# Kernel optimization log

Hardware: AMD Instinct MI355X
Metric: run time of the kernel (lower is better)

## Reference

```python
import jax, jax.numpy as jnp
import numpy as np

N_NODES = 100000   # n_nodes
N_EDGES = 1600000  # n_nodes * avg_degree(16)
D_IN = 128
D_OUT = 128


def setup_inputs() -> dict:
    key = jax.random.key(0)
    k1, k2, k3, k4, k5 = jax.random.split(key, 5)
    h = jax.random.normal(k1, (N_NODES, D_IN), dtype=jnp.float32)
    edge_src = jax.random.randint(k2, (N_EDGES,), 0, N_NODES, dtype=jnp.int32)
    edge_dst = jax.random.randint(k3, (N_EDGES,), 0, N_NODES, dtype=jnp.int32)
    # Linear params, init per reset_parameters: U(-stdv, stdv), stdv = 1/sqrt(in_feats)
    stdv = 1.0 / np.sqrt(D_IN)
    W = jax.random.uniform(k4, (D_OUT, D_IN), dtype=jnp.float32, minval=-stdv, maxval=stdv)
    b = jax.random.uniform(k5, (D_OUT,), dtype=jnp.float32, minval=-stdv, maxval=stdv)
    return {"h": h, "edge_src": edge_src, "edge_dst": edge_dst, "W": W, "b": b}


def reference(h, edge_src, edge_dst, W, b):
    # update_all(copy_src('h'), sum) == neighbor-sum aggregation (SpMM with 0/1 adjacency)
    ah = jax.ops.segment_sum(h[edge_src], edge_dst, num_segments=N_NODES)  # [N, D_IN]
    # dense linear + activation fused on the aggregated features
    return jax.nn.relu(ah @ W.T + b)  # [N, D_OUT]
```

## Files before the change

### kernel.cpp

```cpp
#include <hip/hip_runtime.h>

#define D 128
#define BKT_SHIFT 9
#define BKT_SIZE 512
#define P1_EPB 4096
#define SW_LDU 68

typedef __attribute__((ext_vector_type(8))) short bf16x8;
typedef __attribute__((ext_vector_type(4))) float f32x4;

__device__ inline unsigned int pack2bf(float a, float b) {
    unsigned int ua = __float_as_uint(a);
    unsigned int ub = __float_as_uint(b);
    ua = (ua + 0x7fffu + ((ua >> 16) & 1u)) >> 16;
    ub = (ub + 0x7fffu + ((ub >> 16) & 1u)) >> 16;
    return ua | (ub << 16);
}
__device__ inline unsigned short pack1bf(float a) {
    unsigned int ua = __float_as_uint(a);
    return (unsigned short)((ua + 0x7fffu + ((ua >> 16) & 1u)) >> 16);
}


__global__ __launch_bounds__(256) void p1_partition_kernel(
    const int* __restrict__ esrc, const int* __restrict__ edst,
    int* __restrict__ bucketCur, unsigned int* __restrict__ pairs,
    int n_edges, int cap)
{
    __shared__ int hist[256];
    __shared__ int lbase[256];
    __shared__ int gbase[256];
    __shared__ int cur[256];
    __shared__ unsigned int buf[P1_EPB];
    __shared__ unsigned char bkt8[P1_EPB];
    const int tid = threadIdx.x;
    const int base = blockIdx.x * P1_EPB;
    hist[tid] = 0;
    __syncthreads();
    unsigned int pk[16]; int bk[16];
    #pragma unroll
    for (int k = 0; k < 16; k++) {
        int e = base + k * 256 + tid;
        if (e < n_edges) {
            int sv = esrc[e], dv = edst[e];
            bk[k] = dv >> BKT_SHIFT;
            pk[k] = ((unsigned)sv << BKT_SHIFT) | (unsigned)(dv & (BKT_SIZE - 1));
            atomicAdd(&hist[bk[k]], 1);
        } else bk[k] = -1;
    }
    __syncthreads();
    const int v = hist[tid];
    if (v > 0) {
        int res = atomicAdd(&bucketCur[tid], v);
        if (res > cap) res = cap;
        gbase[tid] = tid * cap + res;
    }
    lbase[tid] = v;
    __syncthreads();
    #pragma unroll
    for (int off = 1; off < 256; off <<= 1) {
        int x = (tid >= off) ? lbase[tid - off] : 0;
        __syncthreads();
        lbase[tid] += x;
        __syncthreads();
    }
    const int excl = lbase[tid] - v;
    __syncthreads();
    lbase[tid] = excl;
    cur[tid] = excl;
    __syncthreads();
    #pragma unroll
    for (int k = 0; k < 16; k++) {
        if (bk[k] >= 0) {
            int loc = atomicAdd(&cur[bk[k]], 1);
            buf[loc] = pk[k];
            bkt8[loc] = (unsigned char)bk[k];
        }
    }
    __syncthreads();
    const int total = min(P1_EPB, n_edges - base);
    for (int i = tid; i < total; i += 256) {
        int b = bkt8[i];
        pairs[(size_t)gbase[b] + (i - lbase[b])] = buf[i];
    }
}

__global__ __launch_bounds__(256) void p2_sort_gemm_kernel(
    const unsigned int* __restrict__ pairs, const int* __restrict__ bucketCur,
    int* __restrict__ sorted_src, int* __restrict__ gstart, int* __restrict__ gend,
    const float* __restrict__ h, const float* __restrict__ W,
    unsigned short* __restrict__ z,
    int n_nodes, int nbk, int cap)
{
    __shared__ union SU {
        struct { int hist[BKT_SIZE]; int cur[BKT_SIZE]; int sb[256]; } s;
        unsigned int sW[128 * SW_LDU];
    } u;
    const int tid = threadIdx.x;

    if ((int)blockIdx.x < nbk) {
        const int bkt = blockIdx.x;
        const int nbase = bkt << BKT_SHIFT;
        const int pstart = bkt * cap;
        int cnt = bucketCur[bkt];
        if (cnt > cap) cnt = cap;
        const int pend = pstart + cnt;
        u.s.hist[tid] = 0; u.s.hist[tid + 256] = 0;
        __syncthreads();
        {
            int j = pstart + tid;
            for (; j + 768 < pend; j += 1024) {
                unsigned int q0 = pairs[j];
                unsigned int q1 = pairs[j + 256];
                unsigned int q2 = pairs[j + 512];
                unsigned int q3 = pairs[j + 768];
                atomicAdd(&u.s.hist[q0 & (BKT_SIZE - 1)], 1);
                atomicAdd(&u.s.hist[q1 & (BKT_SIZE - 1)], 1);
                atomicAdd(&u.s.hist[q2 & (BKT_SIZE - 1)], 1);
                atomicAdd(&u.s.hist[q3 & (BKT_SIZE - 1)], 1);
            }
            for (; j < pend; j += 256)
                atomicAdd(&u.s.hist[pairs[j] & (BKT_SIZE - 1)], 1);
        }
        __syncthreads();
        int a  = u.s.hist[2 * tid];
        int b2 = u.s.hist[2 * tid + 1];
        int psum = a + b2;
        u.s.sb[tid] = psum;
        __syncthreads();
        #pragma unroll
        for (int off = 1; off < 256; off <<= 1) {
            int x = (tid >= off) ? u.s.sb[tid - off] : 0;
            __syncthreads();
            u.s.sb[tid] += x;
            __syncthreads();
        }
        int pexcl = u.s.sb[tid] - psum;
        u.s.cur[2 * tid] = pexcl;
        u.s.cur[2 * tid + 1] = pexcl + a;
        __syncthreads();
        for (int i = tid; i < BKT_SIZE; i += 256) {
            int nd = nbase + i;
            if (nd < n_nodes) {
                int st = pstart + u.s.cur[i];
                gstart[nd] = st;
                gend[nd] = st + u.s.hist[i];
            }
        }
        __syncthreads();
        {
            int j = pstart + tid;
            for (; j + 768 < pend; j += 1024) {
                unsigned int q0 = pairs[j];
                unsigned int q1 = pairs[j + 256];
                unsigned int q2 = pairs[j + 512];
                unsigned int q3 = pairs[j + 768];
                int p0 = pstart + atomicAdd(&u.s.cur[q0 & (BKT_SIZE - 1)], 1);
                int p1 = pstart + atomicAdd(&u.s.cur[q1 & (BKT_SIZE - 1)], 1);
                int p2 = pstart + atomicAdd(&u.s.cur[q2 & (BKT_SIZE - 1)], 1);
                int p3 = pstart + atomicAdd(&u.s.cur[q3 & (BKT_SIZE - 1)], 1);
                sorted_src[p0] = (int)(q0 >> BKT_SHIFT);
                sorted_src[p1] = (int)(q1 >> BKT_SHIFT);
                sorted_src[p2] = (int)(q2 >> BKT_SHIFT);
                sorted_src[p3] = (int)(q3 >> BKT_SHIFT);
            }
            for (; j < pend; j += 256) {
                unsigned int p = pairs[j];
                int local = p & (BKT_SIZE - 1);
                int pos = pstart + atomicAdd(&u.s.cur[local], 1);
                sorted_src[pos] = (int)(p >> BKT_SHIFT);
            }
        }
    } else {
        const int gbid = blockIdx.x - nbk;
        for (int i = tid; i < 4096; i += 256) {
            float4 w = ((const float4*)W)[i];
            int row = i >> 5, c4 = i & 31;
            unsigned int* dst = &u.sW[row * SW_LDU + c4 * 2];
            dst[0] = pack2bf(w.x, w.y);
            dst[1] = pack2bf(w.z, w.w);
        }
        __syncthreads();

        const int wave = tid >> 6;
        const int lane = tid & 63;
        const int m = lane & 15;
        const int q = lane >> 4;
        const int r0 = gbid * 64 + wave * 16;
        const int arow = r0 + m;
        const bool rvalid = arow < n_nodes;

        bf16x8 afrag[4];
        #pragma unroll
        for (int ks = 0; ks < 4; ks++) {
            float4 x = make_float4(0.f, 0.f, 0.f, 0.f), y = x;
            if (rvalid) {
                const float4* p = (const float4*)(h + (size_t)arow * D + ks * 32 + q * 8);
                x = p[0]; y = p[1];
            }
            union { unsigned int uu[4]; bf16x8 v; } cvt;
            cvt.uu[0] = pack2bf(x.x, x.y);
            cvt.uu[1] = pack2bf(x.z, x.w);
            cvt.uu[2] = pack2bf(y.x, y.y);
            cvt.uu[3] = pack2bf(y.z, y.w);
            afrag[ks] = cvt.v;
        }

        f32x4 acc[8];
        #pragma unroll
        for (int ct = 0; ct < 8; ct++) acc[ct] = (f32x4){0.f, 0.f, 0.f, 0.f};

        #pragma unroll
        for (int ct = 0; ct < 8; ct++) {
            #pragma unroll
            for (int ks = 0; ks < 4; ks++) {
                const unsigned int* p = &u.sW[(ct * 16 + m) * SW_LDU + ks * 16 + q * 4];
                union { uint4 uu; bf16x8 v; } bu;
                bu.uu = *(const uint4*)p;
                acc[ct] = __builtin_amdgcn_mfma_f32_16x16x32_bf16(afrag[ks], bu.v, acc[ct], 0, 0, 0);
            }
        }

        __syncthreads();
        unsigned short* lds_us = (unsigned short*)u.sW;
        #pragma unroll
        for (int ct = 0; ct < 8; ct++) {
            #pragma unroll
            for (int i = 0; i < 4; i++) {
                lds_us[(wave * 16 + q * 4 + i) * 130 + ct * 16 + m] = pack1bf(acc[ct][i]);
            }
        }
        __syncthreads();
        const unsigned int* lds32 = (const unsigned int*)u.sW;
        const int r0blk = gbid * 64;
        #pragma unroll
        for (int pass = 0; pass < 4; pass++) {
            int idx = pass * 256 + tid;
            int row = idx >> 4;
            int c16 = idx & 15;
            int r = r0blk + row;
            if (r < n_nodes) {
                int bo = row * 65 + c16 * 4;
                uint4 val;
                val.x = lds32[bo]; val.y = lds32[bo + 1];
                val.z = lds32[bo + 2]; val.w = lds32[bo + 3];
                ((uint4*)z)[(size_t)r * 16 + c16] = val;
            }
        }
    }
}

__global__ __launch_bounds__(256) void gather_row_kernel(
    const unsigned short* __restrict__ z, const int* __restrict__ gstart,
    const int* __restrict__ gend, const int* __restrict__ sorted_src,
    const float* __restrict__ b, float* __restrict__ out, int n_nodes)
{
    const int tid = threadIdx.x;
    const int node = blockIdx.x * 16 + (tid >> 4);
    const int lane = tid & 15;
    if (node >= n_nodes) return;
    int e = gstart[node];
    const int end = gend[node];
    const uint4* __restrict__ z4 = (const uint4*)z;
    float acc[8];
    #pragma unroll
    for (int i = 0; i < 8; i++) acc[i] = 0.f;
#define ADDV(v) do { \
    acc[0] += __uint_as_float((v).x << 16); acc[1] += __uint_as_float((v).x & 0xffff0000u); \
    acc[2] += __uint_as_float((v).y << 16); acc[3] += __uint_as_float((v).y & 0xffff0000u); \
    acc[4] += __uint_as_float((v).z << 16); acc[5] += __uint_as_float((v).z & 0xffff0000u); \
    acc[6] += __uint_as_float((v).w << 16); acc[7] += __uint_as_float((v).w & 0xffff0000u); } while (0)
    for (; e + 4 <= end; e += 4) {
        int s0 = sorted_src[e + 0];
        int s1 = sorted_src[e + 1];
        int s2 = sorted_src[e + 2];
        int s3 = sorted_src[e + 3];
        uint4 v0 = z4[(size_t)s0 * 16 + lane];
        uint4 v1 = z4[(size_t)s1 * 16 + lane];
        uint4 v2 = z4[(size_t)s2 * 16 + lane];
        uint4 v3 = z4[(size_t)s3 * 16 + lane];
        ADDV(v0); ADDV(v1); ADDV(v2); ADDV(v3);
    }
    for (; e < end; e++) {
        uint4 v = z4[(size_t)sorted_src[e] * 16 + lane];
        ADDV(v);
    }
#undef ADDV
    float4 b0 = ((const float4*)b)[lane * 2];
    float4 b1 = ((const float4*)b)[lane * 2 + 1];
    float4* o = (float4*)(out + (size_t)node * D + lane * 8);
    o[0] = make_float4(fmaxf(acc[0] + b0.x, 0.f), fmaxf(acc[1] + b0.y, 0.f),
                       fmaxf(acc[2] + b0.z, 0.f), fmaxf(acc[3] + b0.w, 0.f));
    o[1] = make_float4(fmaxf(acc[4] + b1.x, 0.f), fmaxf(acc[5] + b1.y, 0.f),
                       fmaxf(acc[6] + b1.z, 0.f), fmaxf(acc[7] + b1.w, 0.f));
}


__global__ __launch_bounds__(256) void scatter_kernel(
    const float* __restrict__ h, const int* __restrict__ esrc,
    const int* __restrict__ edst, float* __restrict__ out, int n_edges)
{
    int gid = blockIdx.x * 256 + threadIdx.x;
    int e = gid >> 5;
    int l = gid & 31;
    if (e >= n_edges) return;
    int s = esrc[e];
    int d = edst[e];
    float4 v = ((const float4*)(h + (size_t)s * D))[l];
    float* o = out + (size_t)d * D + (size_t)l * 4;
    atomicAdd(o + 0, v.x);
    atomicAdd(o + 1, v.y);
    atomicAdd(o + 2, v.z);
    atomicAdd(o + 3, v.w);
}

__global__ __launch_bounds__(256) void mfma_gemm_relu_kernel(
    float* __restrict__ io, const float* __restrict__ W,
    const float* __restrict__ b, int n_nodes)
{
    __shared__ unsigned int sW[128 * SW_LDU];
    const int tid = threadIdx.x;
    for (int i = tid; i < 4096; i += 256) {
        float4 w = ((const float4*)W)[i];
        int row = i >> 5, c4 = i & 31;
        unsigned int* dst = &sW[row * SW_LDU + c4 * 2];
        dst[0] = pack2bf(w.x, w.y);
        dst[1] = pack2bf(w.z, w.w);
    }
    __syncthreads();
    const int wave = tid >> 6;
    const int lane = tid & 63;
    const int m = lane & 15;
    const int q = lane >> 4;
    const int r0 = blockIdx.x * 64 + wave * 16;
    const int arow = r0 + m;
    const bool rvalid = arow < n_nodes;
    bf16x8 afrag[4];
    #pragma unroll
    for (int ks = 0; ks < 4; ks++) {
        float4 x = make_float4(0.f, 0.f, 0.f, 0.f), y = x;
        if (rvalid) {
            const float4* p = (const float4*)(io + (size_t)arow * D + ks * 32 + q * 8);
            x = p[0]; y = p[1];
        }
        union { unsigned int u[4]; bf16x8 v; } cvt;
        cvt.u[0] = pack2bf(x.x, x.y);
        cvt.u[1] = pack2bf(x.z, x.w);
        cvt.u[2] = pack2bf(y.x, y.y);
        cvt.u[3] = pack2bf(y.z, y.w);
        afrag[ks] = cvt.v;
    }
    f32x4 acc[8];
    #pragma unroll
    for (int ct = 0; ct < 8; ct++) acc[ct] = (f32x4){0.f, 0.f, 0.f, 0.f};
    #pragma unroll
    for (int ct = 0; ct < 8; ct++) {
        #pragma unroll
        for (int ks = 0; ks < 4; ks++) {
            const unsigned int* p = &sW[(ct * 16 + m) * SW_LDU + ks * 16 + q * 4];
            union { uint4 u; bf16x8 v; } bu;
            bu.u = *(const uint4*)p;
            acc[ct] = __builtin_amdgcn_mfma_f32_16x16x32_bf16(afrag[ks], bu.v, acc[ct], 0, 0, 0);
        }
    }
    #pragma unroll
    for (int ct = 0; ct < 8; ct++) {
        int col = ct * 16 + m;
        float bias = b[col];
        #pragma unroll
        for (int i = 0; i < 4; i++) {
            int r = r0 + q * 4 + i;
            if (r < n_nodes) {
                float v = acc[ct][i] + bias;
                io[(size_t)r * D + col] = v > 0.f ? v : 0.f;
            }
        }
    }
}

extern "C" void kernel_launch(void* const* d_in, const int* in_sizes, int n_in,
                              void* d_out, int out_size, void* d_ws, size_t ws_size,
                              hipStream_t stream) {
    const float* h    = (const float*)d_in[0];
    const int*   esrc = (const int*)d_in[1];
    const int*   edst = (const int*)d_in[2];
    const float* W    = (const float*)d_in[3];
    const float* b    = (const float*)d_in[4];
    float* out = (float*)d_out;
    const int n_nodes = in_sizes[0] / D;
    const int n_edges = in_sizes[1];
    const int NBK = (n_nodes + BKT_SIZE - 1) / BKT_SIZE;

    const int avg = (n_edges + NBK - 1) / NBK;
    const int CAP = (2 * avg + 2047) & ~2047;
    const size_t win = (size_t)NBK * CAP;

    size_t fixed = ((size_t)2 * n_nodes + NBK + 2 * win) * 4;
    size_t z_off = (fixed + 15) & ~(size_t)15;
    size_t need = z_off + (size_t)n_nodes * D * 2;

    if (ws_size >= need && NBK <= 256 && n_nodes <= (1 << 22)) {
        int* gstart     = (int*)d_ws;
        int* gend       = gstart + n_nodes;
        int* bucketCur  = gend + n_nodes;
        int* sorted_src = bucketCur + NBK;
        unsigned int* pairs = (unsigned int*)(sorted_src + win);
        unsigned short* z   = (unsigned short*)((char*)d_ws + z_off);

        hipMemsetAsync(bucketCur, 0, (size_t)NBK * sizeof(int), stream);
        p1_partition_kernel<<<(n_edges + P1_EPB - 1) / P1_EPB, 256, 0, stream>>>(
            esrc, edst, bucketCur, pairs, n_edges, CAP);
        const int gemmBlocks = (n_nodes + 63) / 64;
        p2_sort_gemm_kernel<<<NBK + gemmBlocks, 256, 0, stream>>>(
            pairs, bucketCur, sorted_src, gstart, gend, h, W, z,
            n_nodes, NBK, CAP);
        gather_row_kernel<<<(n_nodes + 15) / 16, 256, 0, stream>>>(
            z, gstart, gend, sorted_src, b, out, n_nodes);
        return;
    }

    hipMemsetAsync(out, 0, (size_t)n_nodes * D * sizeof(float), stream);
    long long total = (long long)n_edges * 32;
    scatter_kernel<<<(int)((total + 255) / 256), 256, 0, stream>>>(h, esrc, edst, out, n_edges);
    mfma_gemm_relu_kernel<<<(n_nodes + 63) / 64, 256, 0, stream>>>(out, W, b, n_nodes);
}
```

Before: 223.3 us.

## Fuse partition, sort/GEMM and gather into one cooperative persistent kernel

Replaces the memset plus three separate kernel launches with a single cooperative persistent kernel that uses grid-wide syncs between the partition, bucket-sort/GEMM and gather phases, with atomic work counters for dynamic scheduling. The aim is to remove launch gaps and tail effects between the stages. In exchange, the grid is limited to resident blocks, the shared-memory union may lower occupancy, and grid.sync adds its own barrier cost. A fallback to the old multi-kernel path remains if cooperative launch is unavailable.

After: 495.5 us. +121.8%, slower.

```diff
diff --git a/kernel.cpp b/kernel.cpp
--- a/kernel.cpp
+++ b/kernel.cpp
@@ -1,4 +1,7 @@
 #include <hip/hip_runtime.h>
+#include <hip/hip_cooperative_groups.h>
+
+namespace cg = cooperative_groups;
 
 #define D 128
 #define BKT_SHIFT 9
@@ -19,6 +22,298 @@
 __device__ inline unsigned short pack1bf(float a) {
     unsigned int ua = __float_as_uint(a);
     return (unsigned short)((ua + 0x7fffu + ((ua >> 16) & 1u)) >> 16);
+}
+
+
+union MegaLDS {
+    struct { int hist[256]; int lbase[256]; int gbase[256]; int cur[256];
+             unsigned int buf[P1_EPB]; unsigned char bkt8[P1_EPB]; } p1;
+    struct { int hist[BKT_SIZE]; int cur[BKT_SIZE]; int sb[256]; } s;
+    unsigned int sW[128 * SW_LDU];
+};
+
+__global__ void mega_kernel(
+    const int* __restrict__ esrc, const int* __restrict__ edst,
+    const float* __restrict__ h, const float* __restrict__ W,
+    const float* __restrict__ b, float* __restrict__ out,
+    int* __restrict__ bucketCur, int* __restrict__ gstart,
+    int* __restrict__ gend, int* __restrict__ sorted_src,
+    unsigned int* __restrict__ pairs, unsigned short* __restrict__ z,
+    int* __restrict__ counters,
+    int n_nodes, int n_edges, int nbk, int cap, int nchunks,
+    int gemmBlocks, int nGather)
+{
+    cg::grid_group grid = cg::this_grid();
+    __shared__ MegaLDS u;
+    __shared__ int s_item;
+    const int tid = threadIdx.x;
+
+    if (blockIdx.x == 0) {
+        if (tid < nbk) bucketCur[tid] = 0;
+        if (tid < 16) counters[tid] = 0;
+    }
+    grid.sync();
+
+    for (int c = blockIdx.x; c < nchunks; c += gridDim.x) {
+        const int base = c * P1_EPB;
+        u.p1.hist[tid] = 0;
+        __syncthreads();
+        unsigned int pk[16]; int bk[16];
+        #pragma unroll
+        for (int k = 0; k < 16; k++) {
+            int e = base + k * 256 + tid;
+            if (e < n_edges) {
+                int sv = esrc[e], dv = edst[e];
+                bk[k] = dv >> BKT_SHIFT;
+                pk[k] = ((unsigned)sv << BKT_SHIFT) | (unsigned)(dv & (BKT_SIZE - 1));
+                atomicAdd(&u.p1.hist[bk[k]], 1);
+            } else bk[k] = -1;
+        }
+        __syncthreads();
+        const int v = u.p1.hist[tid];
+        if (v > 0) {
+            int res = atomicAdd(&bucketCur[tid], v);
+            if (res > cap) res = cap;
+            u.p1.gbase[tid] = tid * cap + res;
+        }
+        u.p1.lbase[tid] = v;
+        __syncthreads();
+        #pragma unroll
+        for (int off = 1; off < 256; off <<= 1) {
+            int x = (tid >= off) ? u.p1.lbase[tid - off] : 0;
+            __syncthreads();
+            u.p1.lbase[tid] += x;
+            __syncthreads();
+        }
+        const int excl = u.p1.lbase[tid] - v;
+        __syncthreads();
+        u.p1.lbase[tid] = excl;
+        u.p1.cur[tid] = excl;
+        __syncthreads();
+        #pragma unroll
+        for (int k = 0; k < 16; k++) {
+            if (bk[k] >= 0) {
+                int loc = atomicAdd(&u.p1.cur[bk[k]], 1);
+                u.p1.buf[loc] = pk[k];
+                u.p1.bkt8[loc] = (unsigned char)bk[k];
+            }
+        }
+        __syncthreads();
+        const int total = min(P1_EPB, n_edges - base);
+        for (int i = tid; i < total; i += 256) {
+            int bb = u.p1.bkt8[i];
+            pairs[(size_t)u.p1.gbase[bb] + (i - u.p1.lbase[bb])] = u.p1.buf[i];
+        }
+        __syncthreads();
+    }
+    grid.sync();
+
+    const int nItems2 = nbk + gemmBlocks;
+    while (true) {
+        __syncthreads();
+        if (tid == 0) s_item = atomicAdd(&counters[0], 1);
+        __syncthreads();
+        const int it = s_item;
+        if (it >= nItems2) break;
+
+        if (it < nbk) {
+            const int bkt = it;
+            const int nbase = bkt << BKT_SHIFT;
+            const int pstart = bkt * cap;
+            int cnt = bucketCur[bkt];
+            if (cnt > cap) cnt = cap;
+            const int pend = pstart + cnt;
+            u.s.hist[tid] = 0; u.s.hist[tid + 256] = 0;
+            __syncthreads();
+            {
+                int j = pstart + tid;
+                for (; j + 768 < pend; j += 1024) {
+                    unsigned int q0 = pairs[j];
+                    unsigned int q1 = pairs[j + 256];
+                    unsigned int q2 = pairs[j + 512];
+                    unsigned int q3 = pairs[j + 768];
+                    atomicAdd(&u.s.hist[q0 & (BKT_SIZE - 1)], 1);
+                    atomicAdd(&u.s.hist[q1 & (BKT_SIZE - 1)], 1);
+                    atomicAdd(&u.s.hist[q2 & (BKT_SIZE - 1)], 1);
+                    atomicAdd(&u.s.hist[q3 & (BKT_SIZE - 1)], 1);
+                }
+                for (; j < pend; j += 256)
+                    atomicAdd(&u.s.hist[pairs[j] & (BKT_SIZE - 1)], 1);
+            }
+            __syncthreads();
+            int a  = u.s.hist[2 * tid];
+            int b2 = u.s.hist[2 * tid + 1];
+            int psum = a + b2;
+            u.s.sb[tid] = psum;
+            __syncthreads();
+            #pragma unroll
+            for (int off = 1; off < 256; off <<= 1) {
+                int x = (tid >= off) ? u.s.sb[tid - off] : 0;
+                __syncthreads();
+                u.s.sb[tid] += x;
+                __syncthreads();
+            }
+            int pexcl = u.s.sb[tid] - psum;
+            u.s.cur[2 * tid] = pexcl;
+            u.s.cur[2 * tid + 1] = pexcl + a;
+            __syncthreads();
+            for (int i = tid; i < BKT_SIZE; i += 256) {
+                int nd = nbase + i;
+                if (nd < n_nodes) {
+                    int st = pstart + u.s.cur[i];
+                    gstart[nd] = st;
+                    gend[nd] = st + u.s.hist[i];
+                }
+            }
+            __syncthreads();
+            {
+                int j = pstart + tid;
+                for (; j + 768 < pend; j += 1024) {
+                    unsigned int q0 = pairs[j];
+                    unsigned int q1 = pairs[j + 256];
+                    unsigned int q2 = pairs[j + 512];
+                    unsigned int q3 = pairs[j + 768];
+                    int p0 = pstart + atomicAdd(&u.s.cur[q0 & (BKT_SIZE - 1)], 1);
+                    int p1 = pstart + atomicAdd(&u.s.cur[q1 & (BKT_SIZE - 1)], 1);
+                    int p2 = pstart + atomicAdd(&u.s.cur[q2 & (BKT_SIZE - 1)], 1);
+                    int p3 = pstart + atomicAdd(&u.s.cur[q3 & (BKT_SIZE - 1)], 1);
+                    sorted_src[p0] = (int)(q0 >> BKT_SHIFT);
+                    sorted_src[p1] = (int)(q1 >> BKT_SHIFT);
+                    sorted_src[p2] = (int)(q2 >> BKT_SHIFT);
+                    sorted_src[p3] = (int)(q3 >> BKT_SHIFT);
+                }
+                for (; j < pend; j += 256) {
+                    unsigned int p = pairs[j];
+                    int local = p & (BKT_SIZE - 1);
+                    int pos = pstart + atomicAdd(&u.s.cur[local], 1);
+                    sorted_src[pos] = (int)(p >> BKT_SHIFT);
+                }
+            }
+        } else {
+            const int gbid = it - nbk;
+            for (int i = tid; i < 4096; i += 256) {
+                float4 w = ((const float4*)W)[i];
+                int row = i >> 5, c4 = i & 31;
+                unsigned int* dst = &u.sW[row * SW_LDU + c4 * 2];
+                dst[0] = pack2bf(w.x, w.y);
+                dst[1] = pack2bf(w.z, w.w);
+            }
+            __syncthreads();
+
+            const int wave = tid >> 6;
+            const int lane = tid & 63;
+            const int m = lane & 15;
+            const int q = lane >> 4;
+            const int r0 = gbid * 64 + wave * 16;
+            const int arow = r0 + m;
+            const bool rvalid = arow < n_nodes;
+
+            bf16x8 afrag[4];
+            #pragma unroll
+            for (int ks = 0; ks < 4; ks++) {
+                float4 x = make_float4(0.f, 0.f, 0.f, 0.f), y = x;
+                if (rvalid) {
+                    const float4* p = (const float4*)(h + (size_t)arow * D + ks * 32 + q * 8);
+                    x = p[0]; y = p[1];
+                }
+                union { unsigned int uu[4]; bf16x8 v; } cvt;
+                cvt.uu[0] = pack2bf(x.x, x.y);
+                cvt.uu[1] = pack2bf(x.z, x.w);
+                cvt.uu[2] = pack2bf(y.x, y.y);
+                cvt.uu[3] = pack2bf(y.z, y.w);
+                afrag[ks] = cvt.v;
+            }
+
+            f32x4 acc[8];
+            #pragma unroll
+            for (int ct = 0; ct < 8; ct++) acc[ct] = (f32x4){0.f, 0.f, 0.f, 0.f};
+
+            #pragma unroll
+            for (int ct = 0; ct < 8; ct++) {
+                #pragma unroll
+                for (int ks = 0; ks < 4; ks++) {
+                    const unsigned int* p = &u.sW[(ct * 16 + m) * SW_LDU + ks * 16 + q * 4];
+                    union { uint4 uu; bf16x8 v; } bu;
+                    bu.uu = *(const uint4*)p;
+                    acc[ct] = __builtin_amdgcn_mfma_f32_16x16x32_bf16(afrag[ks], bu.v, acc[ct], 0, 0, 0);
+                }
+            }
+
+            __syncthreads();
+            unsigned short* lds_us = (unsigned short*)u.sW;
+            #pragma unroll
+            for (int ct = 0; ct < 8; ct++) {
+                #pragma unroll
+                for (int i = 0; i < 4; i++) {
+                    lds_us[(wave * 16 + q * 4 + i) * 130 + ct * 16 + m] = pack1bf(acc[ct][i]);
+                }
+            }
+            __syncthreads();
+            const unsigned int* lds32 = (const unsigned int*)u.sW;
+            const int r0blk = gbid * 64;
+            #pragma unroll
+            for (int pass = 0; pass < 4; pass++) {
+                int idx = pass * 256 + tid;
+                int row = idx >> 4;
+                int c16 = idx & 15;
+                int r = r0blk + row;
+                if (r < n_nodes) {
+                    int bo = row * 65 + c16 * 4;
+                    uint4 val;
+                    val.x = lds32[bo]; val.y = lds32[bo + 1];
+                    val.z = lds32[bo + 2]; val.w = lds32[bo + 3];
+                    ((uint4*)z)[(size_t)r * 16 + c16] = val;
+                }
+            }
+        }
+    }
+    grid.sync();
+
+    const uint4* __restrict__ z4 = (const uint4*)z;
+    while (true) {
+        __syncthreads();
+        if (tid == 0) s_item = atomicAdd(&counters[8], 1);
+        __syncthreads();
+        const int it = s_item;
+        if (it >= nGather) break;
+        const int node = it * 16 + (tid >> 4);
+        const int lane = tid & 15;
+        if (node < n_nodes) {
+            int e = gstart[node];
+            const int end = gend[node];
+            float acc[8];
+            #pragma unroll
+            for (int i = 0; i < 8; i++) acc[i] = 0.f;
+#define ADDV(v) do { \
+    acc[0] += __uint_as_float((v).x << 16); acc[1] += __uint_as_float((v).x & 0xffff0000u); \
+    acc[2] += __uint_as_float((v).y << 16); acc[3] += __uint_as_float((v).y & 0xffff0000u); \
+    acc[4] += __uint_as_float((v).z << 16); acc[5] += __uint_as_float((v).z & 0xffff0000u); \
+    acc[6] += __uint_as_float((v).w << 16); acc[7] += __uint_as_float((v).w & 0xffff0000u); } while (0)
+            for (; e + 4 <= end; e += 4) {
+                int s0 = sorted_src[e + 0];
+                int s1 = sorted_src[e + 1];
+                int s2 = sorted_src[e + 2];
+                int s3 = sorted_src[e + 3];
+                uint4 v0 = z4[(size_t)s0 * 16 + lane];
+                uint4 v1 = z4[(size_t)s1 * 16 + lane];
+                uint4 v2 = z4[(size_t)s2 * 16 + lane];
+                uint4 v3 = z4[(size_t)s3 * 16 + lane];
+                ADDV(v0); ADDV(v1); ADDV(v2); ADDV(v3);
+            }
+            for (; e < end; e++) {
+                uint4 v = z4[(size_t)sorted_src[e] * 16 + lane];
+                ADDV(v);
+            }
+#undef ADDV
+            float4 b0 = ((const float4*)b)[lane * 2];
+            float4 b1 = ((const float4*)b)[lane * 2 + 1];
+            float4* o = (float4*)(out + (size_t)node * D + lane * 8);
+            o[0] = make_float4(fmaxf(acc[0] + b0.x, 0.f), fmaxf(acc[1] + b0.y, 0.f),
+                               fmaxf(acc[2] + b0.z, 0.f), fmaxf(acc[3] + b0.w, 0.f));
+            o[1] = make_float4(fmaxf(acc[4] + b1.x, 0.f), fmaxf(acc[5] + b1.y, 0.f),
+                               fmaxf(acc[6] + b1.z, 0.f), fmaxf(acc[7] + b1.w, 0.f));
+        }
+    }
 }
 
 
@@ -390,12 +685,13 @@
     const int n_nodes = in_sizes[0] / D;
     const int n_edges = in_sizes[1];
     const int NBK = (n_nodes + BKT_SIZE - 1) / BKT_SIZE;
+    const int nchunks = (n_edges + P1_EPB - 1) / P1_EPB;
 
     const int avg = (n_edges + NBK - 1) / NBK;
     const int CAP = (2 * avg + 2047) & ~2047;
     const size_t win = (size_t)NBK * CAP;
 
-    size_t fixed = ((size_t)2 * n_nodes + NBK + 2 * win) * 4;
+    size_t fixed = ((size_t)2 * n_nodes + NBK + 16 + 2 * win) * 4;
     size_t z_off = (fixed + 15) & ~(size_t)15;
     size_t need = z_off + (size_t)n_nodes * D * 2;
 
@@ -403,18 +699,57 @@
         int* gstart     = (int*)d_ws;
         int* gend       = gstart + n_nodes;
         int* bucketCur  = gend + n_nodes;
-        int* sorted_src = bucketCur + NBK;
+        int* counters   = bucketCur + NBK;
+        int* sorted_src = counters + 16;
         unsigned int* pairs = (unsigned int*)(sorted_src + win);
         unsigned short* z   = (unsigned short*)((char*)d_ws + z_off);
 
+        const int gemmBlocks = (n_nodes + 63) / 64;
+        const int nGather = (n_nodes + 15) / 16;
+
+        static int s_coop_grid = -2;
+        if (s_coop_grid == -2) {
+            int nb = 0;
+            hipError_t err = hipOccupancyMaxActiveBlocksPerMultiprocessor(
+                &nb, (const void*)mega_kernel, 256, 0);
+            if (err != hipSuccess || nb < 1) {
+                s_coop_grid = -1;
+            } else {
+                hipDeviceProp_t prop{};
+                int dev = 0;
+                if (hipGetDevice(&dev) == hipSuccess &&
+                    hipGetDeviceProperties(&prop, dev) == hipSuccess &&
+                    prop.multiProcessorCount > 0 &&
+                    prop.cooperativeLaunch)
+                    s_coop_grid = nb * prop.multiProcessorCount;
+                else
+                    s_coop_grid = -1;
+            }
+        }
+
+        if (s_coop_grid >= 64) {
+            int grid = s_coop_grid > 4096 ? 4096 : s_coop_grid;
+            int ne = n_edges, nn = n_nodes, nb = NBK, cp = CAP, nc = nchunks;
+            int gb = gemmBlocks, ng = nGather;
+            void* args[] = {
+                (void*)&esrc, (void*)&edst, (void*)&h, (void*)&W, (void*)&b,
+                (void*)&out, (void*)&bucketCur, (void*)&gstart, (void*)&gend,
+                (void*)&sorted_src, (void*)&pairs, (void*)&z, (void*)&counters,
+                (void*)&nn, (void*)&ne, (void*)&nb, (void*)&cp, (void*)&nc,
+                (void*)&gb, (void*)&ng };
+            if (hipLaunchCooperativeKernel((void*)mega_kernel, dim3(grid),
+                                           dim3(256), args, 0, stream) == hipSuccess)
+                return;
+            s_coop_grid = -1;
+        }
+
         hipMemsetAsync(bucketCur, 0, (size_t)NBK * sizeof(int), stream);
-        p1_partition_kernel<<<(n_edges + P1_EPB - 1) / P1_EPB, 256, 0, stream>>>(
+        p1_partition_kernel<<<nchunks, 256, 0, stream>>>(
             esrc, edst, bucketCur, pairs, n_edges, CAP);
-        const int gemmBlocks = (n_nodes + 63) / 64;
         p2_sort_gemm_kernel<<<NBK + gemmBlocks, 256, 0, stream>>>(
             pairs, bucketCur, sorted_src, gstart, gend, h, W, z,
             n_nodes, NBK, CAP);
-        gather_row_kernel<<<(n_nodes + 15) / 16, 256, 0, stream>>>(
+        gather_row_kernel<<<nGather, 256, 0, stream>>>(
             z, gstart, gend, sorted_src, b, out, n_nodes);
         return;
     }
```

## Co-schedule GEMM with edge partition instead of bucket sort kernel

Applied to the files above, without the earlier changes.

Moves the dense h·W GEMM blocks from the bucket-sort kernel into the edge-partition kernel, and makes the per-bucket counting sort a separate kernel. Stage 2 had only ~196 sort blocks, so the GEMM work now overlaps with the ~391 partition chunks while the sort kernel runs alone. The shared-memory union now covers the partition buffers and the W tile, which may change occupancy. Partition blocks (4096 edges each) and GEMM blocks now compete for compute units in the same launch.

New measurement: 222.7 us. Within noise of the previous version (-0.3%).

```diff
diff --git a/kernel.cpp b/kernel.cpp
--- a/kernel.cpp
+++ b/kernel.cpp
@@ -22,157 +22,72 @@
 }
 
 
-__global__ __launch_bounds__(256) void p1_partition_kernel(
+__global__ __launch_bounds__(256) void p1_gemm_kernel(
     const int* __restrict__ esrc, const int* __restrict__ edst,
     int* __restrict__ bucketCur, unsigned int* __restrict__ pairs,
-    int n_edges, int cap)
-{
-    __shared__ int hist[256];
-    __shared__ int lbase[256];
-    __shared__ int gbase[256];
-    __shared__ int cur[256];
-    __shared__ unsigned int buf[P1_EPB];
-    __shared__ unsigned char bkt8[P1_EPB];
-    const int tid = threadIdx.x;
-    const int base = blockIdx.x * P1_EPB;
-    hist[tid] = 0;
-    __syncthreads();
-    unsigned int pk[16]; int bk[16];
-    #pragma unroll
-    for (int k = 0; k < 16; k++) {
-        int e = base + k * 256 + tid;
-        if (e < n_edges) {
-            int sv = esrc[e], dv = edst[e];
-            bk[k] = dv >> BKT_SHIFT;
-            pk[k] = ((unsigned)sv << BKT_SHIFT) | (unsigned)(dv & (BKT_SIZE - 1));
-            atomicAdd(&hist[bk[k]], 1);
-        } else bk[k] = -1;
-    }
-    __syncthreads();
-    const int v = hist[tid];
-    if (v > 0) {
-        int res = atomicAdd(&bucketCur[tid], v);
-        if (res > cap) res = cap;
-        gbase[tid] = tid * cap + res;
-    }
-    lbase[tid] = v;
-    __syncthreads();
-    #pragma unroll
-    for (int off = 1; off < 256; off <<= 1) {
-        int x = (tid >= off) ? lbase[tid - off] : 0;
-        __syncthreads();
-        lbase[tid] += x;
-        __syncthreads();
-    }
-    const int excl = lbase[tid] - v;
-    __syncthreads();
-    lbase[tid] = excl;
-    cur[tid] = excl;
-    __syncthreads();
-    #pragma unroll
-    for (int k = 0; k < 16; k++) {
-        if (bk[k] >= 0) {
-            int loc = atomicAdd(&cur[bk[k]], 1);
-            buf[loc] = pk[k];
-            bkt8[loc] = (unsigned char)bk[k];
-        }
-    }
-    __syncthreads();
-    const int total = min(P1_EPB, n_edges - base);
-    for (int i = tid; i < total; i += 256) {
-        int b = bkt8[i];
-        pairs[(size_t)gbase[b] + (i - lbase[b])] = buf[i];
-    }
-}
-
-__global__ __launch_bounds__(256) void p2_sort_gemm_kernel(
-    const unsigned int* __restrict__ pairs, const int* __restrict__ bucketCur,
-    int* __restrict__ sorted_src, int* __restrict__ gstart, int* __restrict__ gend,
     const float* __restrict__ h, const float* __restrict__ W,
     unsigned short* __restrict__ z,
-    int n_nodes, int nbk, int cap)
+    int n_edges, int n_nodes, int nchunks, int cap)
 {
-    __shared__ union SU {
-        struct { int hist[BKT_SIZE]; int cur[BKT_SIZE]; int sb[256]; } s;
+    __shared__ union U {
+        struct { int hist[256]; int lbase[256]; int gbase[256]; int cur[256];
+                 unsigned int buf[P1_EPB]; unsigned char bkt8[P1_EPB]; } p1;
         unsigned int sW[128 * SW_LDU];
     } u;
     const int tid = threadIdx.x;
 
-    if ((int)blockIdx.x < nbk) {
-        const int bkt = blockIdx.x;
-        const int nbase = bkt << BKT_SHIFT;
-        const int pstart = bkt * cap;
-        int cnt = bucketCur[bkt];
-        if (cnt > cap) cnt = cap;
-        const int pend = pstart + cnt;
-        u.s.hist[tid] = 0; u.s.hist[tid + 256] = 0;
-        __syncthreads();
-        {
-            int j = pstart + tid;
-            for (; j + 768 < pend; j += 1024) {
-                unsigned int q0 = pairs[j];
-                unsigned int q1 = pairs[j + 256];
-                unsigned int q2 = pairs[j + 512];
-                unsigned int q3 = pairs[j + 768];
-                atomicAdd(&u.s.hist[q0 & (BKT_SIZE - 1)], 1);
-                atomicAdd(&u.s.hist[q1 & (BKT_SIZE - 1)], 1);
-                atomicAdd(&u.s.hist[q2 & (BKT_SIZE - 1)], 1);
-                atomicAdd(&u.s.hist[q3 & (BKT_SIZE - 1)], 1);
-            }
-            for (; j < pend; j += 256)
-                atomicAdd(&u.s.hist[pairs[j] & (BKT_SIZE - 1)], 1);
-        }
-        __syncthreads();
-        int a  = u.s.hist[2 * tid];
-        int b2 = u.s.hist[2 * tid + 1];
-        int psum = a + b2;
-        u.s.sb[tid] = psum;
+    if ((int)blockIdx.x < nchunks) {
+        const int base = blockIdx.x * P1_EPB;
+        u.p1.hist[tid] = 0;
+        __syncthreads();
+        unsigned int pk[16]; int bk[16];
+        #pragma unroll
+        for (int k = 0; k < 16; k++) {
+            int e = base + k * 256 + tid;
+            if (e < n_edges) {
+                int sv = esrc[e], dv = edst[e];
+                bk[k] = dv >> BKT_SHIFT;
+                pk[k] = ((unsigned)sv << BKT_SHIFT) | (unsigned)(dv & (BKT_SIZE - 1));
+                atomicAdd(&u.p1.hist[bk[k]], 1);
+            } else bk[k] = -1;
+        }
+        __syncthreads();
+        const int v = u.p1.hist[tid];
+        if (v > 0) {
+            int res = atomicAdd(&bucketCur[tid], v);
+            if (res > cap) res = cap;
+            u.p1.gbase[tid] = tid * cap + res;
+        }
+        u.p1.lbase[tid] = v;
         __syncthreads();
         #pragma unroll
         for (int off = 1; off < 256; off <<= 1) {
-            int x = (tid >= off) ? u.s.sb[tid - off] : 0;
+            int x = (tid >= off) ? u.p1.lbase[tid - off] : 0;
             __syncthreads();
-            u.s.sb[tid] += x;
+            u.p1.lbase[tid] += x;
             __syncthreads();
         }
-        int pexcl = u.s.sb[tid] - psum;
-        u.s.cur[2 * tid] = pexcl;
-        u.s.cur[2 * tid + 1] = pexcl + a;
-        __syncthreads();
-        for (int i = tid; i < BKT_SIZE; i += 256) {
-            int nd = nbase + i;
-            if (nd < n_nodes) {
-                int st = pstart + u.s.cur[i];
-                gstart[nd] = st;
-                gend[nd] = st + u.s.hist[i];
-            }
-        }
-        __syncthreads();
-        {
-            int j = pstart + tid;
-            for (; j + 768 < pend; j += 1024) {
-                unsigned int q0 = pairs[j];
-                unsigned int q1 = pairs[j + 256];
-                unsigned int q2 = pairs[j + 512];
-                unsigned int q3 = pairs[j + 768];
-                int p0 = pstart + atomicAdd(&u.s.cur[q0 & (BKT_SIZE - 1)], 1);
-                int p1 = pstart + atomicAdd(&u.s.cur[q1 & (BKT_SIZE - 1)], 1);
-                int p2 = pstart + atomicAdd(&u.s.cur[q2 & (BKT_SIZE - 1)], 1);
-                int p3 = pstart + atomicAdd(&u.s.cur[q3 & (BKT_SIZE - 1)], 1);
-                sorted_src[p0] = (int)(q0 >> BKT_SHIFT);
-                sorted_src[p1] = (int)(q1 >> BKT_SHIFT);
-                sorted_src[p2] = (int)(q2 >> BKT_SHIFT);
-                sorted_src[p3] = (int)(q3 >> BKT_SHIFT);
-            }
-            for (; j < pend; j += 256) {
-                unsigned int p = pairs[j];
-                int local = p & (BKT_SIZE - 1);
-                int pos = pstart + atomicAdd(&u.s.cur[local], 1);
-                sorted_src[pos] = (int)(p >> BKT_SHIFT);
-            }
+        const int excl = u.p1.lbase[tid] - v;
+        __syncthreads();
+        u.p1.lbase[tid] = excl;
+        u.p1.cur[tid] = excl;
+        __syncthreads();
+        #pragma unroll
+        for (int k = 0; k < 16; k++) {
+            if (bk[k] >= 0) {
+                int loc = atomicAdd(&u.p1.cur[bk[k]], 1);
+                u.p1.buf[loc] = pk[k];
+                u.p1.bkt8[loc] = (unsigned char)bk[k];
+            }
+        }
+        __syncthreads();
+        const int total = min(P1_EPB, n_edges - base);
+        for (int i = tid; i < total; i += 256) {
+            int b = u.p1.bkt8[i];
+            pairs[(size_t)u.p1.gbase[b] + (i - u.p1.lbase[b])] = u.p1.buf[i];
         }
     } else {
-        const int gbid = blockIdx.x - nbk;
+        const int gbid = blockIdx.x - nchunks;
         for (int i = tid; i < 4096; i += 256) {
             float4 w = ((const float4*)W)[i];
             int row = i >> 5, c4 = i & 31;
@@ -246,6 +161,89 @@
                 val.z = lds32[bo + 2]; val.w = lds32[bo + 3];
                 ((uint4*)z)[(size_t)r * 16 + c16] = val;
             }
+        }
+    }
+}
+
+__global__ __launch_bounds__(256) void p2_sort_kernel(
+    const unsigned int* __restrict__ pairs, const int* __restrict__ bucketCur,
+    int* __restrict__ sorted_src, int* __restrict__ gstart, int* __restrict__ gend,
+    int n_nodes, int nbk, int cap)
+{
+    __shared__ int hist[BKT_SIZE];
+    __shared__ int cur[BKT_SIZE];
+    __shared__ int sb[256];
+    const int tid = threadIdx.x;
+    const int bkt = blockIdx.x;
+    const int nbase = bkt << BKT_SHIFT;
+    const int pstart = bkt * cap;
+    int cnt = bucketCur[bkt];
+    if (cnt > cap) cnt = cap;
+    const int pend = pstart + cnt;
+    hist[tid] = 0; hist[tid + 256] = 0;
+    __syncthreads();
+    {
+        int j = pstart + tid;
+        for (; j + 768 < pend; j += 1024) {
+            unsigned int q0 = pairs[j];
+            unsigned int q1 = pairs[j + 256];
+            unsigned int q2 = pairs[j + 512];
+            unsigned int q3 = pairs[j + 768];
+            atomicAdd(&hist[q0 & (BKT_SIZE - 1)], 1);
+            atomicAdd(&hist[q1 & (BKT_SIZE - 1)], 1);
+            atomicAdd(&hist[q2 & (BKT_SIZE - 1)], 1);
+            atomicAdd(&hist[q3 & (BKT_SIZE - 1)], 1);
+        }
+        for (; j < pend; j += 256)
+            atomicAdd(&hist[pairs[j] & (BKT_SIZE - 1)], 1);
+    }
+    __syncthreads();
+    int a  = hist[2 * tid];
+    int b2 = hist[2 * tid + 1];
+    int psum = a + b2;
+    sb[tid] = psum;
+    __syncthreads();
+    #pragma unroll
+    for (int off = 1; off < 256; off <<= 1) {
+        int x = (tid >= off) ? sb[tid - off] : 0;
+        __syncthreads();
+        sb[tid] += x;
+        __syncthreads();
+    }
+    int pexcl = sb[tid] - psum;
+    cur[2 * tid] = pexcl;
+    cur[2 * tid + 1] = pexcl + a;
+    __syncthreads();
+    for (int i = tid; i < BKT_SIZE; i += 256) {
+        int nd = nbase + i;
+        if (nd < n_nodes) {
+            int st = pstart + cur[i];
+            gstart[nd] = st;
+            gend[nd] = st + hist[i];
+        }
+    }
+    __syncthreads();
+    {
+        int j = pstart + tid;
+        for (; j + 768 < pend; j += 1024) {
+            unsigned int q0 = pairs[j];
+            unsigned int q1 = pairs[j + 256];
+            unsigned int q2 = pairs[j + 512];
+            unsigned int q3 = pairs[j + 768];
+            int p0 = pstart + atomicAdd(&cur[q0 & (BKT_SIZE - 1)], 1);
+            int p1 = pstart + atomicAdd(&cur[q1 & (BKT_SIZE - 1)], 1);
+            int p2 = pstart + atomicAdd(&cur[q2 & (BKT_SIZE - 1)], 1);
+            int p3 = pstart + atomicAdd(&cur[q3 & (BKT_SIZE - 1)], 1);
+            sorted_src[p0] = (int)(q0 >> BKT_SHIFT);
+            sorted_src[p1] = (int)(q1 >> BKT_SHIFT);
+            sorted_src[p2] = (int)(q2 >> BKT_SHIFT);
+            sorted_src[p3] = (int)(q3 >> BKT_SHIFT);
+        }
+        for (; j < pend; j += 256) {
+            unsigned int p = pairs[j];
+            int local = p & (BKT_SIZE - 1);
+            int pos = pstart + atomicAdd(&cur[local], 1);
+            sorted_src[pos] = (int)(p >> BKT_SHIFT);
         }
     }
 }
@@ -390,6 +388,7 @@
     const int n_nodes = in_sizes[0] / D;
     const int n_edges = in_sizes[1];
     const int NBK = (n_nodes + BKT_SIZE - 1) / BKT_SIZE;
+    const int nchunks = (n_edges + P1_EPB - 1) / P1_EPB;
 
     const int avg = (n_edges + NBK - 1) / NBK;
     const int CAP = (2 * avg + 2047) & ~2047;
@@ -407,13 +406,14 @@
         unsigned int* pairs = (unsigned int*)(sorted_src + win);
         unsigned short* z   = (unsigned short*)((char*)d_ws + z_off);
 
+        const int gemmBlocks = (n_nodes + 63) / 64;
+
         hipMemsetAsync(bucketCur, 0, (size_t)NBK * sizeof(int), stream);
-        p1_partition_kernel<<<(n_edges + P1_EPB - 1) / P1_EPB, 256, 0, stream>>>(
-            esrc, edst, bucketCur, pairs, n_edges, CAP);
-        const int gemmBlocks = (n_nodes + 63) / 64;
-        p2_sort_gemm_kernel<<<NBK + gemmBlocks, 256, 0, stream>>>(
-            pairs, bucketCur, sorted_src, gstart, gend, h, W, z,
-            n_nodes, NBK, CAP);
+        p1_gemm_kernel<<<nchunks + gemmBlocks, 256, 0, stream>>>(
+            esrc, edst, bucketCur, pairs, h, W, z,
+            n_edges, n_nodes, nchunks, CAP);
+        p2_sort_kernel<<<NBK, 256, 0, stream>>>(
+            pairs, bucketCur, sorted_src, gstart, gend, n_nodes, NBK, CAP);
         gather_row_kernel<<<(n_nodes + 15) / 16, 256, 0, stream>>>(
             z, gstart, gend, sorted_src, b, out, n_nodes);
         return;
```
